# Kernel optimization log

Measured on AMD Instinct MI355X. Metric: run time of the kernel, lower is better.

The kernel has to match this reference:

```python
import jax, jax.numpy as jnp
import numpy as np

HIDDEN = 2048
N_HEADS = 8
N_KV_HEADS = 1
HEAD_DIM = 256
ROPE_THETA = 10000.0
B, S = 2, 2048


def setup_inputs() -> dict:
    key = jax.random.key(0)
    ks = jax.random.split(key, 6)
    sc = 0.02
    hidden_states = jax.random.normal(ks[0], (B, S, HIDDEN), dtype=jnp.float32)
    position_ids = jnp.broadcast_to(jnp.arange(S, dtype=jnp.int64 if jax.config.jax_enable_x64 else jnp.int32), (B, S))
    # additive causal mask: 0 on/below diagonal, large negative above
    causal = jnp.tril(jnp.ones((S, S), dtype=bool))
    attention_mask = jnp.where(causal, 0.0, -1e9).astype(jnp.float32)[None, None, :, :]
    attention_mask = jnp.broadcast_to(attention_mask, (B, 1, S, S))
    Wq = jax.random.normal(ks[1], (HIDDEN, N_HEADS * HEAD_DIM), dtype=jnp.float32) * sc
    Wk = jax.random.normal(ks[2], (HIDDEN, N_KV_HEADS * HEAD_DIM), dtype=jnp.float32) * sc
    Wv = jax.random.normal(ks[3], (HIDDEN, N_KV_HEADS * HEAD_DIM), dtype=jnp.float32) * sc
    Wo = jax.random.normal(ks[4], (N_HEADS * HEAD_DIM, HIDDEN), dtype=jnp.float32) * sc
    return {"hidden_states": hidden_states, "position_ids": position_ids,
            "attention_mask": attention_mask, "Wq": Wq, "Wk": Wk, "Wv": Wv, "Wo": Wo}


def _rotate_half(x):
    x1, x2 = jnp.split(x, 2, axis=-1)
    return jnp.concatenate([-x2, x1], axis=-1)


def _rope_cos_sin(position_ids, dtype):
    # inv_freq: [head_dim/2]
    inv_freq = 1.0 / (ROPE_THETA ** (jnp.arange(0, HEAD_DIM, 2, dtype=jnp.float32) / HEAD_DIM))
    # freqs: [B, S, head_dim/2]
    freqs = position_ids.astype(jnp.float32)[:, :, None] * inv_freq[None, None, :]
    emb = jnp.concatenate([freqs, freqs], axis=-1)  # [B, S, head_dim]
    return jnp.cos(emb).astype(dtype), jnp.sin(emb).astype(dtype)


def reference(hidden_states, position_ids, attention_mask, Wq, Wk, Wv, Wo):
    b, s, _ = hidden_states.shape
    # projections (bias=False)
    q = (hidden_states @ Wq).reshape(b, s, N_HEADS, HEAD_DIM).transpose(0, 2, 1, 3)      # [B,H,S,D]
    k = (hidden_states @ Wk).reshape(b, s, N_KV_HEADS, HEAD_DIM).transpose(0, 2, 1, 3)   # [B,Hk,S,D]
    v = (hidden_states @ Wv).reshape(b, s, N_KV_HEADS, HEAD_DIM).transpose(0, 2, 1, 3)
    cos, sin = _rope_cos_sin(position_ids, hidden_states.dtype)  # [B,S,D]
    cos, sin = cos[:, None], sin[:, None]  # [B,1,S,D]
    q = q * cos + _rotate_half(q) * sin
    k = k * cos + _rotate_half(k) * sin
    # repeat_kv for GQA
    n_rep = N_HEADS // N_KV_HEADS
    k = jnp.repeat(k, n_rep, axis=1)  # [B,H,S,D]
    v = jnp.repeat(v, n_rep, axis=1)
    scale = HEAD_DIM ** -0.5
    scores = jnp.einsum('bhqd,bhkd->bhqk', q, k) * scale + attention_mask
    attn_weights = jax.nn.softmax(scores.astype(jnp.float32), axis=-1).astype(q.dtype)
    attn_out = jnp.einsum('bhqk,bhkd->bhqd', attn_weights, v)
    attn_out = attn_out.transpose(0, 2, 1, 3).reshape(b, s, N_HEADS * HEAD_DIM)
    out = attn_out @ Wo
    return out, attn_weights
```

## Files before the change

kernel.cpp:

```cpp
#include <hip/hip_runtime.h>
#include <hip/hip_bf16.h>
#include <math.h>

typedef __attribute__((ext_vector_type(4))) float f32x4;
typedef __attribute__((ext_vector_type(8))) __bf16 bf16x8;
typedef __attribute__((ext_vector_type(8))) unsigned short u16x8;

#define HID    2048
#define NHEADS 8
#define HDIM   256
#define SEQ    2048
#define BATCH  2
#define ROWS   (BATCH*SEQ)
#define QKVN   (NHEADS*HDIM + 2*HDIM)
#define NBH    (BATCH*NHEADS)
#define NPTILE 32

#define BIGNEG (-3.0e38f)

typedef __attribute__((address_space(1))) const void gvoid_t;
typedef __attribute__((address_space(3))) void lvoid_t;

__device__ __forceinline__ void gload16(const void* g, void* l){
  __builtin_amdgcn_global_load_lds((gvoid_t*)g, (lvoid_t*)l, 16, 0, 0);
}

__device__ __forceinline__ float bf2f(unsigned short u){
  union { unsigned int i; float f; } x; x.i = ((unsigned int)u) << 16; return x.f;
}
__device__ __forceinline__ unsigned short f2bf(float f){
  union { float f; unsigned int i; } x; x.f = f;
  unsigned int u = x.i;
  return (unsigned short)((u + 0x7FFFu + ((u >> 16) & 1u)) >> 16);
}

__global__ __launch_bounds__(256)
void k_f32_to_bf16(const float* __restrict__ src, unsigned short* __restrict__ dst){
  long i = ((long)blockIdx.x * 256 + threadIdx.x) * 16;
  f32x4 x0 = *(const f32x4*)(src + i);
  f32x4 x1 = *(const f32x4*)(src + i + 4);
  f32x4 x2 = *(const f32x4*)(src + i + 8);
  f32x4 x3 = *(const f32x4*)(src + i + 12);
  u16x8 w0, w1;
  #pragma unroll
  for (int j = 0; j < 4; ++j){
    w0[j]   = f2bf(x0[j]);
    w0[4+j] = f2bf(x1[j]);
    w1[j]   = f2bf(x2[j]);
    w1[4+j] = f2bf(x3[j]);
  }
  *(u16x8*)(dst + i)     = w0;
  *(u16x8*)(dst + i + 8) = w1;
}

__global__ __launch_bounds__(256)
void k_transpose(const float* __restrict__ src, unsigned short* __restrict__ dst,
                 int srcCols, int dstLd){
  __shared__ float t[32][33];
  int bx = blockIdx.x * 32;
  int by = blockIdx.y * 32;
  int tx = threadIdx.x & 31, ty = threadIdx.x >> 5;
  #pragma unroll
  for (int i = 0; i < 4; ++i){
    int rr = ty + i*8;
    t[rr][tx] = src[(long)(by + rr)*srcCols + bx + tx];
  }
  __syncthreads();
  #pragma unroll
  for (int i = 0; i < 4; ++i){
    int rr = ty + i*8;
    dst[(long)(bx + rr)*dstLd + by + tx] = f2bf(t[tx][rr]);
  }
}

__global__ __launch_bounds__(256)
void k_rope(const unsigned short* __restrict__ qkv, const int* __restrict__ pos_ids,
            unsigned short* __restrict__ Qb, unsigned short* __restrict__ Kb,
            unsigned short* __restrict__ VT){
  int row = blockIdx.x;
  int b = row >> 11, s = row & (SEQ - 1);
  float pos = (float)pos_ids[row];
  int tid = threadIdx.x;
  const unsigned short* r = qkv + (long)row * QKVN;

  #pragma unroll
  for (int it = 0; it < 4; ++it){
    int p = it*256 + tid;
    int d = p & 127, h = p >> 7;
    int col = h*HDIM + d;
    float inv = (float)exp((double)d * -0.07195578415606393);
    float ang = pos * inv;
    float sn, cs; sincosf(ang, &sn, &cs);
    float x0 = bf2f(r[col]), x1 = bf2f(r[col + 128]);
    Qb[(long)row*HID + col]       = f2bf(x0*cs - x1*sn);
    Qb[(long)row*HID + col + 128] = f2bf(x1*cs + x0*sn);
  }
  if (tid < 128){
    int d = tid;
    float inv = (float)exp((double)d * -0.07195578415606393);
    float ang = pos * inv;
    float sn, cs; sincosf(ang, &sn, &cs);
    float x0 = bf2f(r[HID + d]), x1 = bf2f(r[HID + d + 128]);
    Kb[(long)row*HDIM + d]       = f2bf(x0*cs - x1*sn);
    Kb[(long)row*HDIM + d + 128] = f2bf(x1*cs + x0*sn);
  }
  {
    int d = tid;
    VT[((long)b*HDIM + d)*SEQ + s] = r[HID + HDIM + d];
  }
}

__global__ __launch_bounds__(256)
void k_pvsm(float* __restrict__ S, const unsigned short* __restrict__ VT,
            unsigned short* __restrict__ AOb, const float* __restrict__ part){
  constexpr int QB = 32, BK = 64;
  int bh = blockIdx.x; int b = bh >> 3, h = bh & 7;
  int qtile = 63 - (int)blockIdx.z;
  int qbase = qtile * QB;
  int kceil = (qbase & ~63) + 64;
  int iters = kceil >> 6;

  float* Sh = S + (long)bh * SEQ * SEQ;
  const unsigned short* Vb = VT + (long)b * HDIM * SEQ;
  const float* pmb = part + (long)bh * NPTILE * SEQ;
  const float* plb = pmb + (long)NBH * NPTILE * SEQ;

  __shared__ unsigned short lA[QB*BK];
  __shared__ unsigned short lB[2*HDIM*BK];
  __shared__ float mlm[QB], mli[QB];

  int tid = threadIdx.x, lane = tid & 63, w = tid >> 6;
  int prow = tid >> 3, c8 = tid & 7;
  int vswz = ((lane & 7) ^ ((lane >> 3) & 7)) * 8;

  {
    int r = qbase + prow;
    float m = BIGNEG, l = 0.f;
    int nt = (r >> 6) + 1;
    for (int tc = c8; tc < nt; tc += 8){
      float mt = pmb[(long)tc*SEQ + r], lt = plb[(long)tc*SEQ + r];
      float nm = fmaxf(m, mt);
      l = l*__expf(m - nm) + lt*__expf(mt - nm);
      m = nm;
    }
    #pragma unroll
    for (int off = 1; off < 8; off <<= 1){
      float om = __shfl_xor(m, off), ol = __shfl_xor(l, off);
      float nm = fmaxf(m, om);
      l = l*__expf(m - nm) + ol*__expf(om - nm);
      m = nm;
    }
    if (c8 == 0){ mlm[prow] = m; mli[prow] = 1.0f / l; }
  }
  __syncthreads();

  float pm  = mlm[prow];
  float pil = mli[prow];
  int   rglob = qbase + prow;
  float* prowp = Sh + (long)rglob * SEQ;

  f32x4 acc[2][4];
  #pragma unroll
  for (int m = 0; m < 2; ++m)
    #pragma unroll
    for (int n = 0; n < 4; ++n)
      #pragma unroll
      for (int q = 0; q < 4; ++q) acc[m][n][q] = 0.f;

#define STAGE_V(k0_, buf_)                                                     \
  { _Pragma("unroll")                                                          \
    for (int t = 0; t < 8; ++t){                                               \
      int seg = w*8 + t;                                                       \
      const unsigned short* src = Vb + (long)(seg*8 + (lane >> 3))*SEQ + (k0_) + vswz; \
      gload16(src, (char*)lB + (buf_)*32768 + seg*1024);                       \
    } }

  f32x4 x0 = *(const f32x4*)(prowp + c8*8);
  f32x4 x1 = *(const f32x4*)(prowp + c8*8 + 4);
  STAGE_V(0, 0)
  int cur = 0;

  for (int it = 0; it < iters; ++it){
    int k0 = it * BK;
    asm volatile("s_waitcnt vmcnt(8)" ::: "memory");
    u16x8 u; f32x4 y0, y1;
    #pragma unroll
    for (int j = 0; j < 4; ++j){
      float p0 = (k0 + c8*8 + j     <= rglob) ? __expf(x0[j] - pm) * pil : 0.f;
      float p1 = (k0 + c8*8 + 4 + j <= rglob) ? __expf(x1[j] - pm) * pil : 0.f;
      y0[j] = p0; y1[j] = p1;
      u[j] = f2bf(p0); u[4+j] = f2bf(p1);
    }
    *(f32x4*)(prowp + k0 + c8*8)     = y0;
    *(f32x4*)(prowp + k0 + c8*8 + 4) = y1;
    { int kb = (c8*16) ^ ((prow & 7) << 4);
      *(u16x8*)((char*)lA + prow*128 + kb) = u; }
    if (it + 1 < iters){
      int k1 = k0 + BK;
      x0 = *(const f32x4*)(prowp + k1 + c8*8);
      x1 = *(const f32x4*)(prowp + k1 + c8*8 + 4);
      STAGE_V(k1, cur^1)
      asm volatile("s_waitcnt vmcnt(12)" ::: "memory");
    } else {
      asm volatile("s_waitcnt vmcnt(2)" ::: "memory");
    }
    asm volatile("s_waitcnt lgkmcnt(0)" ::: "memory");
    __builtin_amdgcn_s_barrier();

    const char* lBc = (const char*)lB + cur*32768;
    __builtin_amdgcn_s_setprio(1);
    #pragma unroll
    for (int kk = 0; kk < 2; ++kk){
      bf16x8 af[2];
      #pragma unroll
      for (int m = 0; m < 2; ++m){
        int row = m*16 + (lane & 15);
        int kb = (kk*64 + (lane >> 4)*16) ^ ((row & 7) << 4);
        af[m] = *(const bf16x8*)((const char*)lA + row*128 + kb);
      }
      #pragma unroll
      for (int n = 0; n < 4; ++n){
        int vr = w*64 + n*16 + (lane & 15);
        int kb = (kk*64 + (lane >> 4)*16) ^ ((vr & 7) << 4);
        bf16x8 bfr = *(const bf16x8*)(lBc + vr*128 + kb);
        acc[0][n] = __builtin_amdgcn_mfma_f32_16x16x32_bf16(af[0], bfr, acc[0][n], 0, 0, 0);
        acc[1][n] = __builtin_amdgcn_mfma_f32_16x16x32_bf16(af[1], bfr, acc[1][n], 0, 0, 0);
      }
    }
    __builtin_amdgcn_s_setprio(0);
    __builtin_amdgcn_s_barrier();
    cur ^= 1;
  }
#undef STAGE_V

  {
    f32x4 z4; z4[0]=0.f; z4[1]=0.f; z4[2]=0.f; z4[3]=0.f;
    for (int c0 = kceil; c0 < SEQ; c0 += BK){
      *(f32x4*)(prowp + c0 + c8*8)     = z4;
      *(f32x4*)(prowp + c0 + c8*8 + 4) = z4;
    }
  }

  #pragma unroll
  for (int m = 0; m < 2; ++m){
    #pragma unroll
    for (int ri = 0; ri < 4; ++ri){
      int row = qbase + m*16 + (lane >> 4)*4 + ri;
      long gr = (long)b*SEQ + row;
      #pragma unroll
      for (int n = 0; n < 4; ++n){
        int col = w*64 + n*16 + (lane & 15);
        AOb[gr*HID + h*HDIM + col] = f2bf(acc[m][n][ri]);
      }
    }
  }
}

template<int OUTF32>
__global__ __launch_bounds__(512, 1)
void gemm256(const unsigned short* __restrict__ A16, const unsigned short* __restrict__ BT,
             void* __restrict__ Cv, int lda, int ldb, int ldc, int K){
  constexpr int BM = 256, BN = 128, BK = 64;
  int m0 = blockIdx.x * BM, n0 = blockIdx.y * BN;

  __shared__ unsigned short lA[2][BM*BK];
  __shared__ unsigned short lB[2][BN*BK];

  int tid = threadIdx.x, lane = tid & 63, w = tid >> 6;
  int wr = w >> 1, wc = w & 1;
  int srow = lane >> 3;
  int vswz = ((lane & 7) ^ ((lane >> 3) & 7)) * 8;

  f32x4 acc[4][4];
  #pragma unroll
  for (int m = 0; m < 4; ++m)
    #pragma unroll
    for (int n = 0; n < 4; ++n)
      #pragma unroll
      for (int q = 0; q < 4; ++q) acc[m][n][q] = 0.f;

  int NT = K / BK;

#define STAGE256(kt_, buf_)                                                    \
  { int k0_ = (kt_) * BK;                                                      \
    _Pragma("unroll")                                                          \
    for (int t = 0; t < 4; ++t){                                               \
      int seg = w*4 + t;                                                       \
      const unsigned short* src = A16 + (long)(m0 + seg*8 + srow)*lda + k0_ + vswz; \
      gload16(src, (char*)lA[buf_] + seg*1024);                                \
    }                                                                          \
    _Pragma("unroll")                                                          \
    for (int t = 0; t < 2; ++t){                                               \
      int seg = w*2 + t;                                                       \
      const unsigned short* src = BT + (long)(n0 + seg*8 + srow)*ldb + k0_ + vswz; \
      gload16(src, (char*)lB[buf_] + seg*1024);                                \
    } }

  STAGE256(0, 0)
  STAGE256(1, 1)
  int cur = 0;

  for (int kt = 0; kt < NT; ++kt){
    if (kt < NT - 1) asm volatile("s_waitcnt vmcnt(6)" ::: "memory");
    else             asm volatile("s_waitcnt vmcnt(0)" ::: "memory");
    __builtin_amdgcn_s_barrier();

    const char* La = (const char*)lA[cur];
    const char* Lb = (const char*)lB[cur];
    __builtin_amdgcn_s_setprio(1);
    #pragma unroll
    for (int kk = 0; kk < 2; ++kk){
      bf16x8 af[4], bfr[4];
      #pragma unroll
      for (int m = 0; m < 4; ++m){
        int row = wr*64 + m*16 + (lane & 15);
        int kb = (kk*64 + (lane >> 4)*16) ^ ((row & 7) << 4);
        af[m] = *(const bf16x8*)(La + row*128 + kb);
      }
      #pragma unroll
      for (int n = 0; n < 4; ++n){
        int row = wc*64 + n*16 + (lane & 15);
        int kb = (kk*64 + (lane >> 4)*16) ^ ((row & 7) << 4);
        bfr[n] = *(const bf16x8*)(Lb + row*128 + kb);
      }
      #pragma unroll
      for (int m = 0; m < 4; ++m)
        #pragma unroll
        for (int n = 0; n < 4; ++n)
          acc[m][n] = __builtin_amdgcn_mfma_f32_16x16x32_bf16(af[m], bfr[n], acc[m][n], 0, 0, 0);
    }
    __builtin_amdgcn_s_setprio(0);
    __builtin_amdgcn_s_barrier();
    if (kt + 2 < NT) STAGE256(kt + 2, cur)
    cur ^= 1;
  }
#undef STAGE256

  #pragma unroll
  for (int m = 0; m < 4; ++m){
    #pragma unroll
    for (int ri = 0; ri < 4; ++ri){
      int orow = m0 + wr*64 + m*16 + (lane >> 4)*4 + ri;
      #pragma unroll
      for (int n = 0; n < 4; ++n){
        int ocol = n0 + wc*64 + n*16 + (lane & 15);
        float vv = acc[m][n][ri];
        if (OUTF32) ((float*)Cv)[(long)orow*ldc + ocol] = vv;
        else        ((unsigned short*)Cv)[(long)orow*ldc + ocol] = f2bf(vv);
      }
    }
  }
}

__global__ __launch_bounds__(256)
void gemm_scores(const unsigned short* __restrict__ Qb, const unsigned short* __restrict__ Kb,
                 float* __restrict__ Cv, float* __restrict__ part, float scale){
  constexpr int BM = 128, BN = 128, BK = 32;
  int m0 = blockIdx.x * BM, n0 = blockIdx.y * BN;
  if (n0 > m0 + BM - 1) return;

  int z = blockIdx.z;
  int zb = z >> 3;

  const unsigned short* A16 = Qb + (long)zb*SEQ*HID + (long)(z & 7)*HDIM;
  const unsigned short* BT  = Kb + (long)zb*SEQ*HDIM;

  __shared__ unsigned short lA[BM*BK];
  __shared__ unsigned short lB[BN*BK];

  int tid = threadIdx.x, lane = tid & 63, w = tid >> 6;
  int wr = w >> 1, wc = w & 1;
  int lrow = lane & 15, lk = (lane >> 4) * 8;

  f32x4 acc[4][4];
  #pragma unroll
  for (int m = 0; m < 4; ++m)
    #pragma unroll
    for (int n = 0; n < 4; ++n)
      #pragma unroll
      for (int q = 0; q < 4; ++q) acc[m][n][q] = 0.f;

  for (int k0 = 0; k0 < HDIM; k0 += BK){
    #pragma unroll
    for (int t = 0; t < 2; ++t){
      int seg = w*2 + t;
      const unsigned short* src = A16 + (long)(m0 + seg*16 + (lane >> 2))*HID + k0 + (lane & 3)*8;
      gload16(src, &lA[seg*512]);
    }
    #pragma unroll
    for (int t = 0; t < 2; ++t){
      int seg = w*2 + t;
      const unsigned short* src = BT + (long)(n0 + seg*16 + (lane >> 2))*HDIM + k0 + (lane & 3)*8;
      gload16(src, &lB[seg*512]);
    }
    __syncthreads();

    bf16x8 af[4], bfr[4];
    #pragma unroll
    for (int m = 0; m < 4; ++m)
      af[m] = *(const bf16x8*)&lA[(wr*64 + m*16 + lrow)*BK + lk];
    #pragma unroll
    for (int n = 0; n < 4; ++n)
      bfr[n] = *(const bf16x8*)&lB[(wc*64 + n*16 + lrow)*BK + lk];
    #pragma unroll
    for (int m = 0; m < 4; ++m)
      #pragma unroll
      for (int n = 0; n < 4; ++n)
        acc[m][n] = __builtin_amdgcn_mfma_f32_16x16x32_bf16(af[m], bfr[n], acc[m][n], 0, 0, 0);
    __syncthreads();
  }

  long cbase = (long)z * SEQ * SEQ;
  int tc = (n0 + wc*64) >> 6;
  float* pm_out = part + ((long)z * NPTILE + tc) * SEQ;
  float* pl_out = pm_out + (long)NBH * NPTILE * SEQ;
  #pragma unroll
  for (int m = 0; m < 4; ++m){
    #pragma unroll
    for (int ri = 0; ri < 4; ++ri){
      int orow = m0 + wr*64 + m*16 + (lane >> 4)*4 + ri;
      float v[4]; bool ok[4];
      float mx = BIGNEG;
      #pragma unroll
      for (int n = 0; n < 4; ++n){
        int ocol = n0 + wc*64 + n*16 + (lane & 15);
        v[n] = acc[m][n][ri] * scale;
        ok[n] = (ocol <= orow);
        if (ok[n]){
          Cv[cbase + (long)orow*SEQ + ocol] = v[n];
          mx = fmaxf(mx, v[n]);
        }
      }
      #pragma unroll
      for (int off = 8; off; off >>= 1) mx = fmaxf(mx, __shfl_xor(mx, off));
      float sm = 0.f;
      #pragma unroll
      for (int n = 0; n < 4; ++n) if (ok[n]) sm += __expf(v[n] - mx);
      #pragma unroll
      for (int off = 8; off; off >>= 1) sm += __shfl_xor(sm, off);
      if ((lane & 15) == 0){ pm_out[orow] = mx; pl_out[orow] = sm; }
    }
  }
}

extern "C" void kernel_launch(void* const* d_in, const int* in_sizes, int n_in,
                              void* d_out, int out_size, void* d_ws, size_t ws_size,
                              hipStream_t stream){
  const float* hs  = (const float*)d_in[0];
  const int*   pos = (const int*)  d_in[1];
  const float* Wq  = (const float*)d_in[3];
  const float* Wk  = (const float*)d_in[4];
  const float* Wv  = (const float*)d_in[5];
  const float* Wo  = (const float*)d_in[6];

  float* out  = (float*)d_out;
  float* Sbuf = out + (long)ROWS * HID;

  unsigned short* wsp   = (unsigned short*)d_ws;
  unsigned short* hsb   = wsp;
  unsigned short* wqkvT = hsb   + (long)ROWS*HID;
  unsigned short* woT   = wqkvT + (long)QKVN*HID;
  unsigned short* qkvb  = woT   + (long)HID*HID;
  unsigned short* Qb    = qkvb  + (long)ROWS*QKVN;
  unsigned short* Kb    = Qb    + (long)ROWS*HID;
  unsigned short* VT    = Kb    + (long)ROWS*HDIM;
  unsigned short* AOb   = VT    + (long)BATCH*HDIM*SEQ;

  float* part = (float*)hsb;

  k_f32_to_bf16<<<(ROWS*HID)/(256*16), 256, 0, stream>>>(hs, hsb);
  k_transpose<<<dim3(HID/32,  HID/32), 256, 0, stream>>>(Wq, wqkvT, HID, HID);
  k_transpose<<<dim3(HDIM/32, HID/32), 256, 0, stream>>>(Wk, wqkvT + (long)HID*HID, HDIM, HID);
  k_transpose<<<dim3(HDIM/32, HID/32), 256, 0, stream>>>(Wv, wqkvT + (long)(HID+HDIM)*HID, HDIM, HID);
  k_transpose<<<dim3(HID/32,  HID/32), 256, 0, stream>>>(Wo, woT, HID, HID);

  gemm256<0><<<dim3(ROWS/256, QKVN/128), 512, 0, stream>>>(
      hsb, wqkvT, qkvb, HID, HID, QKVN, HID);

  k_rope<<<ROWS, 256, 0, stream>>>(qkvb, pos, Qb, Kb, VT);

  gemm_scores<<<dim3(SEQ/128, SEQ/128, NBH), 256, 0, stream>>>(
      Qb, Kb, Sbuf, part, 0.0625f);

  k_pvsm<<<dim3(NBH, 1, 64), 256, 0, stream>>>(Sbuf, VT, AOb, part);

  gemm256<1><<<dim3(ROWS/256, HID/128), 512, 0, stream>>>(
      AOb, woT, out, HID, HID, HID, HID);
}
```

Measured before the change: 376.1 us.

## Move V transpose to tiled kernel, drop LDS V staging, zero-fill upper scores in GEMM

V transposition moves out of the per-row rope kernel into a dedicated shared-memory tiled transpose kernel, which should give coalesced writes. The PV kernel no longer double-buffers V in LDS through async global-to-LDS loads. It reads V fragments straight from global memory (relying on cache) with plain syncthreads, and gets launch bounds of 4 blocks per CU for occupancy. Zero-filling the masked upper triangle of the score/attention-weights buffer moves from the PV kernel into the scores GEMM, covering both skipped tiles and masked elements. The trade is lost LDS reuse and software pipelining of V loads for reduced LDS use and higher occupancy.

```diff
diff --git a/kernel.cpp b/kernel.cpp
--- a/kernel.cpp
+++ b/kernel.cpp
@@ -75,10 +75,8 @@
 
 __global__ __launch_bounds__(256)
 void k_rope(const unsigned short* __restrict__ qkv, const int* __restrict__ pos_ids,
-            unsigned short* __restrict__ Qb, unsigned short* __restrict__ Kb,
-            unsigned short* __restrict__ VT){
+            unsigned short* __restrict__ Qb, unsigned short* __restrict__ Kb){
   int row = blockIdx.x;
-  int b = row >> 11, s = row & (SEQ - 1);
   float pos = (float)pos_ids[row];
   int tid = threadIdx.x;
   const unsigned short* r = qkv + (long)row * QKVN;
@@ -104,13 +102,27 @@
     Kb[(long)row*HDIM + d]       = f2bf(x0*cs - x1*sn);
     Kb[(long)row*HDIM + d + 128] = f2bf(x1*cs + x0*sn);
   }
-  {
-    int d = tid;
-    VT[((long)b*HDIM + d)*SEQ + s] = r[HID + HDIM + d];
-  }
 }
 
 __global__ __launch_bounds__(256)
+void k_vt(const unsigned short* __restrict__ qkvb, unsigned short* __restrict__ VT){
+  __shared__ unsigned short t[32][34];
+  int d0 = blockIdx.x * 32, s0 = blockIdx.y * 32, b = blockIdx.z;
+  int tx = threadIdx.x & 31, ty = threadIdx.x >> 5;
+  #pragma unroll
+  for (int i = 0; i < 4; ++i){
+    int rr = ty + i*8;
+    t[rr][tx] = qkvb[(long)(b*SEQ + s0 + rr)*QKVN + HID + HDIM + d0 + tx];
+  }
+  __syncthreads();
+  #pragma unroll
+  for (int i = 0; i < 4; ++i){
+    int dd = ty + i*8;
+    VT[((long)b*HDIM + d0 + dd)*SEQ + s0 + tx] = t[tx][dd];
+  }
+}
+
+__global__ __launch_bounds__(256, 4)
 void k_pvsm(float* __restrict__ S, const unsigned short* __restrict__ VT,
             unsigned short* __restrict__ AOb, const float* __restrict__ part){
   constexpr int QB = 32, BK = 64;
@@ -121,17 +133,14 @@
   int iters = kceil >> 6;
 
   float* Sh = S + (long)bh * SEQ * SEQ;
-  const unsigned short* Vb = VT + (long)b * HDIM * SEQ;
   const float* pmb = part + (long)bh * NPTILE * SEQ;
   const float* plb = pmb + (long)NBH * NPTILE * SEQ;
 
   __shared__ unsigned short lA[QB*BK];
-  __shared__ unsigned short lB[2*HDIM*BK];
   __shared__ float mlm[QB], mli[QB];
 
   int tid = threadIdx.x, lane = tid & 63, w = tid >> 6;
   int prow = tid >> 3, c8 = tid & 7;
-  int vswz = ((lane & 7) ^ ((lane >> 3) & 7)) * 8;
 
   {
     int r = qbase + prow;
@@ -159,6 +168,8 @@
   int   rglob = qbase + prow;
   float* prowp = Sh + (long)rglob * SEQ;
 
+  const unsigned short* vb = VT + ((long)b*HDIM + w*64 + (lane & 15))*SEQ + (lane >> 4)*8;
+
   f32x4 acc[2][4];
   #pragma unroll
   for (int m = 0; m < 2; ++m)
@@ -166,23 +177,12 @@
     for (int n = 0; n < 4; ++n)
       #pragma unroll
       for (int q = 0; q < 4; ++q) acc[m][n][q] = 0.f;
-
-#define STAGE_V(k0_, buf_)                                                     \
-  { _Pragma("unroll")                                                          \
-    for (int t = 0; t < 8; ++t){                                               \
-      int seg = w*8 + t;                                                       \
-      const unsigned short* src = Vb + (long)(seg*8 + (lane >> 3))*SEQ + (k0_) + vswz; \
-      gload16(src, (char*)lB + (buf_)*32768 + seg*1024);                       \
-    } }
 
   f32x4 x0 = *(const f32x4*)(prowp + c8*8);
   f32x4 x1 = *(const f32x4*)(prowp + c8*8 + 4);
-  STAGE_V(0, 0)
-  int cur = 0;
 
   for (int it = 0; it < iters; ++it){
     int k0 = it * BK;
-    asm volatile("s_waitcnt vmcnt(8)" ::: "memory");
     u16x8 u; f32x4 y0, y1;
     #pragma unroll
     for (int j = 0; j < 4; ++j){
@@ -191,54 +191,32 @@
       y0[j] = p0; y1[j] = p1;
       u[j] = f2bf(p0); u[4+j] = f2bf(p1);
     }
+    { int kb = (c8*16) ^ ((prow & 7) << 4);
+      *(u16x8*)((char*)lA + prow*128 + kb) = u; }
+    __syncthreads();
+
     *(f32x4*)(prowp + k0 + c8*8)     = y0;
     *(f32x4*)(prowp + k0 + c8*8 + 4) = y1;
-    { int kb = (c8*16) ^ ((prow & 7) << 4);
-      *(u16x8*)((char*)lA + prow*128 + kb) = u; }
     if (it + 1 < iters){
-      int k1 = k0 + BK;
-      x0 = *(const f32x4*)(prowp + k1 + c8*8);
-      x1 = *(const f32x4*)(prowp + k1 + c8*8 + 4);
-      STAGE_V(k1, cur^1)
-      asm volatile("s_waitcnt vmcnt(12)" ::: "memory");
-    } else {
-      asm volatile("s_waitcnt vmcnt(2)" ::: "memory");
-    }
-    asm volatile("s_waitcnt lgkmcnt(0)" ::: "memory");
-    __builtin_amdgcn_s_barrier();
-
-    const char* lBc = (const char*)lB + cur*32768;
-    __builtin_amdgcn_s_setprio(1);
+      x0 = *(const f32x4*)(prowp + k0 + BK + c8*8);
+      x1 = *(const f32x4*)(prowp + k0 + BK + c8*8 + 4);
+    }
+
     #pragma unroll
     for (int kk = 0; kk < 2; ++kk){
-      bf16x8 af[2];
-      #pragma unroll
-      for (int m = 0; m < 2; ++m){
-        int row = m*16 + (lane & 15);
-        int kb = (kk*64 + (lane >> 4)*16) ^ ((row & 7) << 4);
-        af[m] = *(const bf16x8*)((const char*)lA + row*128 + kb);
-      }
+      bf16x8 af0, af1;
+      { int row = (lane & 15);
+        int kb2 = (kk*64 + (lane >> 4)*16) ^ ((row & 7) << 4);
+        af0 = *(const bf16x8*)((const char*)lA + row*128 + kb2);
+        af1 = *(const bf16x8*)((const char*)lA + (row+16)*128 + kb2); }
       #pragma unroll
       for (int n = 0; n < 4; ++n){
-        int vr = w*64 + n*16 + (lane & 15);
-        int kb = (kk*64 + (lane >> 4)*16) ^ ((vr & 7) << 4);
-        bf16x8 bfr = *(const bf16x8*)(lBc + vr*128 + kb);
-        acc[0][n] = __builtin_amdgcn_mfma_f32_16x16x32_bf16(af[0], bfr, acc[0][n], 0, 0, 0);
-        acc[1][n] = __builtin_amdgcn_mfma_f32_16x16x32_bf16(af[1], bfr, acc[1][n], 0, 0, 0);
-      }
-    }
-    __builtin_amdgcn_s_setprio(0);
-    __builtin_amdgcn_s_barrier();
-    cur ^= 1;
-  }
-#undef STAGE_V
-
-  {
-    f32x4 z4; z4[0]=0.f; z4[1]=0.f; z4[2]=0.f; z4[3]=0.f;
-    for (int c0 = kceil; c0 < SEQ; c0 += BK){
-      *(f32x4*)(prowp + c0 + c8*8)     = z4;
-      *(f32x4*)(prowp + c0 + c8*8 + 4) = z4;
-    }
+        bf16x8 bfr = *(const bf16x8*)(vb + (long)n*16*SEQ + k0 + kk*32);
+        acc[0][n] = __builtin_amdgcn_mfma_f32_16x16x32_bf16(af0, bfr, acc[0][n], 0, 0, 0);
+        acc[1][n] = __builtin_amdgcn_mfma_f32_16x16x32_bf16(af1, bfr, acc[1][n], 0, 0, 0);
+      }
+    }
+    __syncthreads();
   }
 
   #pragma unroll
@@ -357,18 +335,25 @@
                  float* __restrict__ Cv, float* __restrict__ part, float scale){
   constexpr int BM = 128, BN = 128, BK = 32;
   int m0 = blockIdx.x * BM, n0 = blockIdx.y * BN;
-  if (n0 > m0 + BM - 1) return;
-
   int z = blockIdx.z;
+  int tid = threadIdx.x;
+
+  if (n0 > m0 + BM - 1){
+    long cb = (long)z*SEQ*SEQ + (long)(m0 + (tid >> 1))*SEQ + n0 + (tid & 1)*64;
+    f32x4 z4; z4[0]=0.f; z4[1]=0.f; z4[2]=0.f; z4[3]=0.f;
+    #pragma unroll
+    for (int j = 0; j < 16; ++j) *(f32x4*)(&Cv[cb + j*4]) = z4;
+    return;
+  }
+
   int zb = z >> 3;
-
   const unsigned short* A16 = Qb + (long)zb*SEQ*HID + (long)(z & 7)*HDIM;
   const unsigned short* BT  = Kb + (long)zb*SEQ*HDIM;
 
   __shared__ unsigned short lA[BM*BK];
   __shared__ unsigned short lB[BN*BK];
 
-  int tid = threadIdx.x, lane = tid & 63, w = tid >> 6;
+  int lane = tid & 63, w = tid >> 6;
   int wr = w >> 1, wc = w & 1;
   int lrow = lane & 15, lk = (lane >> 4) * 8;
 
@@ -426,10 +411,8 @@
         int ocol = n0 + wc*64 + n*16 + (lane & 15);
         v[n] = acc[m][n][ri] * scale;
         ok[n] = (ocol <= orow);
-        if (ok[n]){
-          Cv[cbase + (long)orow*SEQ + ocol] = v[n];
-          mx = fmaxf(mx, v[n]);
-        }
+        Cv[cbase + (long)orow*SEQ + ocol] = ok[n] ? v[n] : 0.f;
+        if (ok[n]) mx = fmaxf(mx, v[n]);
       }
       #pragma unroll
       for (int off = 8; off; off >>= 1) mx = fmaxf(mx, __shfl_xor(mx, off));
@@ -477,7 +460,8 @@
   gemm256<0><<<dim3(ROWS/256, QKVN/128), 512, 0, stream>>>(
       hsb, wqkvT, qkvb, HID, HID, QKVN, HID);
 
-  k_rope<<<ROWS, 256, 0, stream>>>(qkvb, pos, Qb, Kb, VT);
+  k_rope<<<ROWS, 256, 0, stream>>>(qkvb, pos, Qb, Kb);
+  k_vt<<<dim3(HDIM/32, SEQ/32, BATCH), 256, 0, stream>>>(qkvb, VT);
 
   gemm_scores<<<dim3(SEQ/128, SEQ/128, NBH), 256, 0, stream>>>(
       Qb, Kb, Sbuf, part, 0.0625f);
```

After: 419.7 us. 11.6% more time.
